# Kernel optimization log

Measured on AMD Instinct MI355X. Metric: run time of the kernel, lower is better.

## Reference

```python
import jax, jax.numpy as jnp
import numpy as np
from jax.ops import segment_sum

N_NODES = 50000


def gcn_conv(x, W, b, src, dst, num_nodes):
    # PyG GCNConv: add self-loops, symmetric normalization, aggregate at dst (col).
    loop = jnp.arange(num_nodes, dtype=src.dtype)
    src2 = jnp.concatenate([src, loop])
    dst2 = jnp.concatenate([dst, loop])
    deg = segment_sum(jnp.ones_like(dst2, dtype=x.dtype), dst2, num_segments=num_nodes)
    dis = jnp.where(deg > 0, jax.lax.rsqrt(deg), 0.0)
    norm = dis[src2] * dis[dst2]                      # [E+N]
    h = x @ W                                         # [N, out]
    msg = h[src2] * norm[:, None]                     # gather + scale
    out = segment_sum(msg, dst2, num_segments=num_nodes)  # scatter-add
    return out + b


def setup_inputs() -> dict:
    key = jax.random.key(0)
    k = jax.random.split(key, 8)
    E = 600000
    x = jax.random.normal(k[0], (N_NODES, 3), dtype=jnp.float32)
    edge_index = jax.random.randint(k[1], (2, E), 0, N_NODES, dtype=jnp.int64)
    # glorot-ish params
    W1 = jax.random.normal(k[2], (3, 128), dtype=jnp.float32) * (1.0 / np.sqrt(3))
    b1 = jnp.zeros((128,), dtype=jnp.float32)
    W2 = jax.random.normal(k[3], (128, 64), dtype=jnp.float32) * (1.0 / np.sqrt(128))
    b2 = jnp.zeros((64,), dtype=jnp.float32)
    Wfc = jax.random.normal(k[4], (64, 3), dtype=jnp.float32) * (1.0 / np.sqrt(64))
    bfc = jnp.zeros((3,), dtype=jnp.float32)
    return {"x": x, "edge_index": edge_index, "W1": W1, "b1": b1,
            "W2": W2, "b2": b2, "Wfc": Wfc, "bfc": bfc}


def reference(x, edge_index, W1, b1, W2, b2, Wfc, bfc):
    src, dst = edge_index[0], edge_index[1]
    h = jax.nn.relu(gcn_conv(x, W1, b1, src, dst, N_NODES))
    h = jax.nn.relu(gcn_conv(h, W2, b2, src, dst, N_NODES))
    g = jnp.mean(h, axis=0)          # mean pool over nodes -> [64]
    return g @ Wfc + bfc             # [3]
```

## Files before the change

### kernel.cpp

```cpp
#include <hip/hip_runtime.h>

#define NXCD 8
#define BKT 64

__global__ void k_zero(int4* __restrict__ p, int nwords4) {
    int i = blockIdx.x * blockDim.x + threadIdx.x;
    if (i < nwords4) p[i] = make_int4(0, 0, 0, 0);
}

__global__ void k_bucket(const int* __restrict__ src, const int* __restrict__ dst,
                         int* __restrict__ cnt, int* __restrict__ eidx,
                         int E, int nprg, int n) {
    int grp = blockIdx.x & (NXCD - 1);
    int lo = grp * nprg;
    int hi = min(lo + nprg, n);
    int bIn = blockIdx.x >> 3;
    int nBIn = gridDim.x >> 3;
    const int4* dst4 = (const int4*)dst;
    const int4* src4 = (const int4*)src;
    int E4 = E >> 2;
    for (int idx = bIn * blockDim.x + threadIdx.x; idx < E4; idx += nBIn * blockDim.x) {
        int4 d = dst4[idx];
        int4 s = src4[idx];
        if (d.x >= lo && d.x < hi) { int pos = atomicAdd(&cnt[d.x], 1); eidx[(size_t)d.x * BKT + pos] = s.x; }
        if (d.y >= lo && d.y < hi) { int pos = atomicAdd(&cnt[d.y], 1); eidx[(size_t)d.y * BKT + pos] = s.y; }
        if (d.z >= lo && d.z < hi) { int pos = atomicAdd(&cnt[d.z], 1); eidx[(size_t)d.z * BKT + pos] = s.z; }
        if (d.w >= lo && d.w < hi) { int pos = atomicAdd(&cnt[d.w], 1); eidx[(size_t)d.w * BKT + pos] = s.w; }
    }
    if (bIn == 0 && threadIdx.x < (E & 3)) {
        int e = (E4 << 2) + threadIdx.x;
        int d = dst[e];
        if (d >= lo && d < hi) { int pos = atomicAdd(&cnt[d], 1); eidx[(size_t)d * BKT + pos] = src[e]; }
    }
}

__global__ void k_prep(const int* __restrict__ cnt, const float* __restrict__ x,
                       float* __restrict__ dis, float4* __restrict__ xs4, int n) {
    int i = blockIdx.x * blockDim.x + threadIdx.x;
    if (i < n) {
        float d = rsqrtf((float)cnt[i] + 1.0f);
        dis[i] = d;
        xs4[i] = make_float4(x[3 * i + 0] * d, x[3 * i + 1] * d, x[3 * i + 2] * d, 0.f);
    }
}

__global__ __launch_bounds__(256) void k_mlp(const float4* __restrict__ xs4,
                                             const float* __restrict__ dis,
                                             const int* __restrict__ cnt,
                                             const int* __restrict__ eidx,
                                             const float* __restrict__ W1,
                                             const float* __restrict__ b1,
                                             const float* __restrict__ W2,
                                             unsigned* __restrict__ ts, int n) {
    __shared__ float sA0[64], sA1[64], sA2[64];
    __shared__ float sW1[3 * 128];
    __shared__ float sb1[128];
    __shared__ float sHT[64][64];
    __shared__ float sW2[64][64];

    int tid = threadIdx.x;
    int i0 = blockIdx.x * 64;
    if (tid < 128) {
        sW1[tid]       = W1[tid];
        sW1[128 + tid] = W1[128 + tid];
        sW1[256 + tid] = W1[256 + tid];
        sb1[tid]       = b1[tid];
    }

    {
        int nd = tid >> 2;
        int sub = tid & 3;
        int i = i0 + nd;
        float a0 = 0.f, a1 = 0.f, a2 = 0.f;
        if (i < n) {
            int deg = cnt[i];
            const int* ep = eidx + (size_t)i * BKT;
            for (int p = sub; p < deg; p += 4) {
                float4 vs = xs4[ep[p]];
                a0 += vs.x; a1 += vs.y; a2 += vs.z;
            }
        }
        #pragma unroll
        for (int m = 2; m; m >>= 1) {
            a0 += __shfl_xor(a0, m);
            a1 += __shfl_xor(a1, m);
            a2 += __shfl_xor(a2, m);
        }
        if (sub == 0) {
            if (i < n) {
                float di = dis[i];
                float4 vi = xs4[i];
                sA0[nd] = di * (a0 + vi.x);
                sA1[nd] = di * (a1 + vi.y);
                sA2[nd] = di * (a2 + vi.z);
            } else {
                sA0[nd] = 0.f; sA1[nd] = 0.f; sA2[nd] = 0.f;
            }
        }
    }
    __syncthreads();

    int tx = tid & 15, ty = tid >> 4;
    int nn0 = ty * 4, f0 = tx * 4;
    float acc[4][4] = {};

    for (int c = 0; c < 2; ++c) {
        #pragma unroll
        for (int j = 0; j < 16; ++j) {
            int idx = tid + 256 * j;
            int kl = idx >> 6, nd = idx & 63;
            int k = c * 64 + kl;
            float h = fmaf(sA0[nd], sW1[k],
                      fmaf(sA1[nd], sW1[128 + k],
                      fmaf(sA2[nd], sW1[256 + k], sb1[k])));
            sHT[kl][nd] = fmaxf(h, 0.f);
        }
        const float4* W2c = (const float4*)(W2 + c * 64 * 64);
        float4* sW2v = (float4*)sW2;
        #pragma unroll
        for (int j = 0; j < 4; ++j) sW2v[tid + 256 * j] = W2c[tid + 256 * j];
        __syncthreads();

        #pragma unroll 8
        for (int kl = 0; kl < 64; ++kl) {
            float4 hv = *(const float4*)&sHT[kl][nn0];
            float4 wv = *(const float4*)&sW2[kl][f0];
            acc[0][0] = fmaf(hv.x, wv.x, acc[0][0]);
            acc[0][1] = fmaf(hv.x, wv.y, acc[0][1]);
            acc[0][2] = fmaf(hv.x, wv.z, acc[0][2]);
            acc[0][3] = fmaf(hv.x, wv.w, acc[0][3]);
            acc[1][0] = fmaf(hv.y, wv.x, acc[1][0]);
            acc[1][1] = fmaf(hv.y, wv.y, acc[1][1]);
            acc[1][2] = fmaf(hv.y, wv.z, acc[1][2]);
            acc[1][3] = fmaf(hv.y, wv.w, acc[1][3]);
            acc[2][0] = fmaf(hv.z, wv.x, acc[2][0]);
            acc[2][1] = fmaf(hv.z, wv.y, acc[2][1]);
            acc[2][2] = fmaf(hv.z, wv.z, acc[2][2]);
            acc[2][3] = fmaf(hv.z, wv.w, acc[2][3]);
            acc[3][0] = fmaf(hv.w, wv.x, acc[3][0]);
            acc[3][1] = fmaf(hv.w, wv.y, acc[3][1]);
            acc[3][2] = fmaf(hv.w, wv.z, acc[3][2]);
            acc[3][3] = fmaf(hv.w, wv.w, acc[3][3]);
        }
        __syncthreads();
    }

    #pragma unroll
    for (int nn = 0; nn < 4; ++nn) {
        int i = i0 + nn0 + nn;
        if (i < n) {
            float di = dis[i];
            unsigned r = __builtin_amdgcn_cvt_pk_fp8_f32(acc[nn][0] * di, acc[nn][1] * di, 0, false);
            r = __builtin_amdgcn_cvt_pk_fp8_f32(acc[nn][2] * di, acc[nn][3] * di, r, true);
            ts[(size_t)i * 16 + tx] = r;
        }
    }
}

__global__ void k_gather2(const int* __restrict__ cnt, const int* __restrict__ eidx,
                          const unsigned* __restrict__ ts, const float* __restrict__ dis,
                          const float* __restrict__ b2, float* __restrict__ gacc, int n) {
    __shared__ float sred[256 * 4];
    int tid = threadIdx.x;
    int fl = tid & 15;
    int gid = blockIdx.x * (blockDim.x >> 4) + (tid >> 4);
    int ng = gridDim.x * (blockDim.x >> 4);
    float4 b2v = ((const float4*)b2)[fl];
    float4 accg = make_float4(0.f, 0.f, 0.f, 0.f);

    for (int i = gid; i < n; i += ng) {
        unsigned sv = ts[(size_t)i * 16 + fl];
        float4 acc = make_float4(__builtin_amdgcn_cvt_f32_fp8(sv, 0),
                                 __builtin_amdgcn_cvt_f32_fp8(sv, 1),
                                 __builtin_amdgcn_cvt_f32_fp8(sv, 2),
                                 __builtin_amdgcn_cvt_f32_fp8(sv, 3));
        int deg = cnt[i];
        const int* ep = eidx + (size_t)i * BKT;
        int p = 0;
        for (; p + 7 < deg; p += 8) {
            int s0 = ep[p],     s1 = ep[p + 1], s2 = ep[p + 2], s3 = ep[p + 3];
            int s4 = ep[p + 4], s5 = ep[p + 5], s6 = ep[p + 6], s7 = ep[p + 7];
            unsigned a = ts[(size_t)s0 * 16 + fl];
            unsigned b = ts[(size_t)s1 * 16 + fl];
            unsigned c = ts[(size_t)s2 * 16 + fl];
            unsigned d = ts[(size_t)s3 * 16 + fl];
            unsigned e = ts[(size_t)s4 * 16 + fl];
            unsigned f = ts[(size_t)s5 * 16 + fl];
            unsigned g = ts[(size_t)s6 * 16 + fl];
            unsigned h = ts[(size_t)s7 * 16 + fl];
            acc.x += __builtin_amdgcn_cvt_f32_fp8(a, 0) + __builtin_amdgcn_cvt_f32_fp8(b, 0)
                   + __builtin_amdgcn_cvt_f32_fp8(c, 0) + __builtin_amdgcn_cvt_f32_fp8(d, 0)
                   + __builtin_amdgcn_cvt_f32_fp8(e, 0) + __builtin_amdgcn_cvt_f32_fp8(f, 0)
                   + __builtin_amdgcn_cvt_f32_fp8(g, 0) + __builtin_amdgcn_cvt_f32_fp8(h, 0);
            acc.y += __builtin_amdgcn_cvt_f32_fp8(a, 1) + __builtin_amdgcn_cvt_f32_fp8(b, 1)
                   + __builtin_amdgcn_cvt_f32_fp8(c, 1) + __builtin_amdgcn_cvt_f32_fp8(d, 1)
                   + __builtin_amdgcn_cvt_f32_fp8(e, 1) + __builtin_amdgcn_cvt_f32_fp8(f, 1)
                   + __builtin_amdgcn_cvt_f32_fp8(g, 1) + __builtin_amdgcn_cvt_f32_fp8(h, 1);
            acc.z += __builtin_amdgcn_cvt_f32_fp8(a, 2) + __builtin_amdgcn_cvt_f32_fp8(b, 2)
                   + __builtin_amdgcn_cvt_f32_fp8(c, 2) + __builtin_amdgcn_cvt_f32_fp8(d, 2)
                   + __builtin_amdgcn_cvt_f32_fp8(e, 2) + __builtin_amdgcn_cvt_f32_fp8(f, 2)
                   + __builtin_amdgcn_cvt_f32_fp8(g, 2) + __builtin_amdgcn_cvt_f32_fp8(h, 2);
            acc.w += __builtin_amdgcn_cvt_f32_fp8(a, 3) + __builtin_amdgcn_cvt_f32_fp8(b, 3)
                   + __builtin_amdgcn_cvt_f32_fp8(c, 3) + __builtin_amdgcn_cvt_f32_fp8(d, 3)
                   + __builtin_amdgcn_cvt_f32_fp8(e, 3) + __builtin_amdgcn_cvt_f32_fp8(f, 3)
                   + __builtin_amdgcn_cvt_f32_fp8(g, 3) + __builtin_amdgcn_cvt_f32_fp8(h, 3);
        }
        for (; p + 3 < deg; p += 4) {
            int s0 = ep[p], s1 = ep[p + 1], s2 = ep[p + 2], s3 = ep[p + 3];
            unsigned a = ts[(size_t)s0 * 16 + fl];
            unsigned b = ts[(size_t)s1 * 16 + fl];
            unsigned c = ts[(size_t)s2 * 16 + fl];
            unsigned d = ts[(size_t)s3 * 16 + fl];
            acc.x += __builtin_amdgcn_cvt_f32_fp8(a, 0) + __builtin_amdgcn_cvt_f32_fp8(b, 0)
                   + __builtin_amdgcn_cvt_f32_fp8(c, 0) + __builtin_amdgcn_cvt_f32_fp8(d, 0);
            acc.y += __builtin_amdgcn_cvt_f32_fp8(a, 1) + __builtin_amdgcn_cvt_f32_fp8(b, 1)
                   + __builtin_amdgcn_cvt_f32_fp8(c, 1) + __builtin_amdgcn_cvt_f32_fp8(d, 1);
            acc.z += __builtin_amdgcn_cvt_f32_fp8(a, 2) + __builtin_amdgcn_cvt_f32_fp8(b, 2)
                   + __builtin_amdgcn_cvt_f32_fp8(c, 2) + __builtin_amdgcn_cvt_f32_fp8(d, 2);
            acc.w += __builtin_amdgcn_cvt_f32_fp8(a, 3) + __builtin_amdgcn_cvt_f32_fp8(b, 3)
                   + __builtin_amdgcn_cvt_f32_fp8(c, 3) + __builtin_amdgcn_cvt_f32_fp8(d, 3);
        }
        for (; p < deg; ++p) {
            unsigned a = ts[(size_t)ep[p] * 16 + fl];
            acc.x += __builtin_amdgcn_cvt_f32_fp8(a, 0);
            acc.y += __builtin_amdgcn_cvt_f32_fp8(a, 1);
            acc.z += __builtin_amdgcn_cvt_f32_fp8(a, 2);
            acc.w += __builtin_amdgcn_cvt_f32_fp8(a, 3);
        }
        float di = dis[i];
        accg.x += fmaxf(fmaf(acc.x, di, b2v.x), 0.f);
        accg.y += fmaxf(fmaf(acc.y, di, b2v.y), 0.f);
        accg.z += fmaxf(fmaf(acc.z, di, b2v.z), 0.f);
        accg.w += fmaxf(fmaf(acc.w, di, b2v.w), 0.f);
    }

    sred[tid * 4 + 0] = accg.x;
    sred[tid * 4 + 1] = accg.y;
    sred[tid * 4 + 2] = accg.z;
    sred[tid * 4 + 3] = accg.w;
    __syncthreads();
    if (tid < 64) {
        float v = 0.f;
        #pragma unroll
        for (int g = 0; g < 16; ++g) v += sred[g * 64 + tid];
        atomicAdd(&gacc[tid], v);
    }
}

__global__ void k_final(const float* __restrict__ g_accum, const float* __restrict__ Wfc,
                        const float* __restrict__ bfc, float* __restrict__ out, float inv_n) {
    int lane = threadIdx.x;
    float gk = g_accum[lane] * inv_n;
    #pragma unroll
    for (int c = 0; c < 3; ++c) {
        float p = gk * Wfc[lane * 3 + c];
        #pragma unroll
        for (int off = 32; off > 0; off >>= 1) p += __shfl_down(p, off);
        if (lane == 0) out[c] = p + bfc[c];
    }
}

extern "C" void kernel_launch(void* const* d_in, const int* in_sizes, int n_in,
                              void* d_out, int out_size, void* d_ws, size_t ws_size,
                              hipStream_t stream) {
    const float* x   = (const float*)d_in[0];
    const int*   ei  = (const int*)d_in[1];
    const float* W1  = (const float*)d_in[2];
    const float* b1  = (const float*)d_in[3];
    const float* W2  = (const float*)d_in[4];
    const float* b2  = (const float*)d_in[5];
    const float* Wfc = (const float*)d_in[6];
    const float* bfc = (const float*)d_in[7];

    const int N = in_sizes[0] / 3;
    const int E = in_sizes[1] / 2;
    const int* src = ei;
    const int* dst = ei + E;
    const int NPRG = (N + NXCD - 1) / NXCD;

    float* ws = (float*)d_ws;
    float* dis   = ws;
    int*   cnt   = (int*)(ws + (size_t)N);
    float* gacc  = ws + (size_t)2 * N;
    float4* xs4  = (float4*)(ws + (size_t)2 * N + 64);
    int*   eidx  = (int*)(ws + (size_t)6 * N + 64);
    unsigned* ts = (unsigned*)(ws + (size_t)70 * N + 64);

    int nwords4 = (N + 64) / 4;
    k_zero<<<(nwords4 + 255) / 256, 256, 0, stream>>>((int4*)cnt, nwords4);

    k_bucket<<<2048, 256, 0, stream>>>(src, dst, cnt, eidx, E, NPRG, N);
    k_prep<<<(N + 255) / 256, 256, 0, stream>>>(cnt, x, dis, xs4, N);
    k_mlp<<<(N + 63) / 64, 256, 0, stream>>>(xs4, dis, cnt, eidx, W1, b1, W2, ts, N);
    k_gather2<<<2048, 256, 0, stream>>>(cnt, eidx, ts, dis, b2, gacc, N);
    k_final<<<1, 64, 0, stream>>>(gacc, Wfc, bfc, (float*)d_out, 1.0f / (float)N);
}
```

Baseline: 102.1 us.

## Pre-partition edges into per-XCD bins before bucketing by destination

The single bucketing kernel, where each of 8 XCD groups scanned the whole edge list and kept only its own destination range, is replaced by two passes. The first bins edges into 8 coarse partitions using shared-memory counters and one global atomic per block. The second lets each XCD group read only its own bin and do the per-node atomic bucketing. This removes the 8x redundant reading of src/dst, but adds an extra kernel launch and a write plus read of an int2 bin buffer. It also relies on a fixed BINCAP capacity per bin.

```diff
diff --git a/kernel.cpp b/kernel.cpp
--- a/kernel.cpp
+++ b/kernel.cpp
@@ -2,35 +2,51 @@
 
 #define NXCD 8
 #define BKT 64
+#define BINCAP 93752
 
 __global__ void k_zero(int4* __restrict__ p, int nwords4) {
     int i = blockIdx.x * blockDim.x + threadIdx.x;
     if (i < nwords4) p[i] = make_int4(0, 0, 0, 0);
 }
 
-__global__ void k_bucket(const int* __restrict__ src, const int* __restrict__ dst,
-                         int* __restrict__ cnt, int* __restrict__ eidx,
-                         int E, int nprg, int n) {
+__global__ void k_bin(const int* __restrict__ src, const int* __restrict__ dst,
+                      int* __restrict__ bincnt, int2* __restrict__ bins,
+                      int E, int nprg) {
+    __shared__ int sh[NXCD];
+    __shared__ int sbase[NXCD];
+    int tid = threadIdx.x;
+    if (tid < NXCD) sh[tid] = 0;
+    __syncthreads();
+    int chunk = (E + gridDim.x - 1) / gridDim.x;
+    int e0 = blockIdx.x * chunk;
+    int e1 = min(e0 + chunk, E);
+    for (int e = e0 + tid; e < e1; e += 256)
+        atomicAdd(&sh[dst[e] / nprg], 1);
+    __syncthreads();
+    if (tid < NXCD) {
+        sbase[tid] = atomicAdd(&bincnt[tid], sh[tid]);
+        sh[tid] = 0;
+    }
+    __syncthreads();
+    for (int e = e0 + tid; e < e1; e += 256) {
+        int d = dst[e];
+        int b = d / nprg;
+        int pos = sbase[b] + atomicAdd(&sh[b], 1);
+        bins[(size_t)b * BINCAP + pos] = make_int2(src[e], d);
+    }
+}
+
+__global__ void k_bucket2(const int2* __restrict__ bins, const int* __restrict__ bincnt,
+                          int* __restrict__ cnt, int* __restrict__ eidx) {
     int grp = blockIdx.x & (NXCD - 1);
-    int lo = grp * nprg;
-    int hi = min(lo + nprg, n);
     int bIn = blockIdx.x >> 3;
     int nBIn = gridDim.x >> 3;
-    const int4* dst4 = (const int4*)dst;
-    const int4* src4 = (const int4*)src;
-    int E4 = E >> 2;
-    for (int idx = bIn * blockDim.x + threadIdx.x; idx < E4; idx += nBIn * blockDim.x) {
-        int4 d = dst4[idx];
-        int4 s = src4[idx];
-        if (d.x >= lo && d.x < hi) { int pos = atomicAdd(&cnt[d.x], 1); eidx[(size_t)d.x * BKT + pos] = s.x; }
-        if (d.y >= lo && d.y < hi) { int pos = atomicAdd(&cnt[d.y], 1); eidx[(size_t)d.y * BKT + pos] = s.y; }
-        if (d.z >= lo && d.z < hi) { int pos = atomicAdd(&cnt[d.z], 1); eidx[(size_t)d.z * BKT + pos] = s.z; }
-        if (d.w >= lo && d.w < hi) { int pos = atomicAdd(&cnt[d.w], 1); eidx[(size_t)d.w * BKT + pos] = s.w; }
-    }
-    if (bIn == 0 && threadIdx.x < (E & 3)) {
-        int e = (E4 << 2) + threadIdx.x;
-        int d = dst[e];
-        if (d >= lo && d < hi) { int pos = atomicAdd(&cnt[d], 1); eidx[(size_t)d * BKT + pos] = src[e]; }
+    int m = bincnt[grp];
+    const int2* bp = bins + (size_t)grp * BINCAP;
+    for (int i = bIn * 256 + threadIdx.x; i < m; i += nBIn * 256) {
+        int2 e = bp[i];
+        int pos = atomicAdd(&cnt[e.y], 1);
+        eidx[(size_t)e.y * BKT + pos] = e.x;
     }
 }
 
@@ -279,17 +295,20 @@
     const int NPRG = (N + NXCD - 1) / NXCD;
 
     float* ws = (float*)d_ws;
-    float* dis   = ws;
-    int*   cnt   = (int*)(ws + (size_t)N);
-    float* gacc  = ws + (size_t)2 * N;
-    float4* xs4  = (float4*)(ws + (size_t)2 * N + 64);
-    int*   eidx  = (int*)(ws + (size_t)6 * N + 64);
-    unsigned* ts = (unsigned*)(ws + (size_t)70 * N + 64);
-
-    int nwords4 = (N + 64) / 4;
+    float* dis    = ws;
+    int*   cnt    = (int*)(ws + (size_t)N);
+    float* gacc   = ws + (size_t)2 * N;
+    int*   bincnt = (int*)(ws + (size_t)2 * N + 64);
+    float4* xs4   = (float4*)(ws + (size_t)2 * N + 72);
+    int*   eidx   = (int*)(ws + (size_t)6 * N + 72);
+    unsigned* ts  = (unsigned*)(ws + (size_t)70 * N + 72);
+    int2*  bins   = (int2*)(ws + (size_t)86 * N + 72);
+
+    int nwords4 = (N + 72) / 4;
     k_zero<<<(nwords4 + 255) / 256, 256, 0, stream>>>((int4*)cnt, nwords4);
 
-    k_bucket<<<2048, 256, 0, stream>>>(src, dst, cnt, eidx, E, NPRG, N);
+    k_bin<<<2048, 256, 0, stream>>>(src, dst, bincnt, bins, E, NPRG);
+    k_bucket2<<<2048, 256, 0, stream>>>(bins, bincnt, cnt, eidx);
     k_prep<<<(N + 255) / 256, 256, 0, stream>>>(cnt, x, dis, xs4, N);
     k_mlp<<<(N + 63) / 64, 256, 0, stream>>>(xs4, dis, cnt, eidx, W1, b1, W2, ts, N);
     k_gather2<<<2048, 256, 0, stream>>>(cnt, eidx, ts, dis, b2, gacc, N);
```

Result: slower. 129.3 us (+26.6%).
